# Optimization experiments

Measured on AMD Instinct MI355X. Metric: run time of the kernel, lower is better.

## Reference

```python
import jax, jax.numpy as jnp
import numpy as np

B, S, V, D, H, L, C = 64, 128, 50000, 300, 128, 20, 3
EPS = 1e-8


def lstm(x, w_ih, w_hh, b):
    # x: (B,S,D) -> outputs (B,S,H); torch gate order i,f,g,o
    xg = jnp.einsum('bsd,gd->bsg', x, w_ih) + b  # (B,S,4H)
    Hh = w_hh.shape[1]

    def step(carry, xt):
        hprev, cprev = carry
        g = xt + hprev @ w_hh.T
        i, f, gg, o = jnp.split(g, 4, axis=-1)
        c = jax.nn.sigmoid(f) * cprev + jax.nn.sigmoid(i) * jnp.tanh(gg)
        hnew = jax.nn.sigmoid(o) * jnp.tanh(c)
        return (hnew, c), hnew

    z = jnp.zeros((x.shape[0], Hh), x.dtype)
    _, hs = jax.lax.scan(step, (z, z), xg.transpose(1, 0, 2))
    return hs.transpose(1, 0, 2)


def bilstm(x, wih_f, whh_f, b_f, wih_b, whh_b, b_b):
    fwd = lstm(x, wih_f, whh_f, b_f)
    bwd = jnp.flip(lstm(jnp.flip(x, 1), wih_b, whh_b, b_b), 1)
    return jnp.concatenate([fwd, bwd], axis=-1)


def safe_div(prod, norm):
    # matches module's cosine_similarity eps handling
    return prod / jnp.where(norm > EPS, norm, EPS)


def full_matching(p1, p2, w):
    # p1: (B,S,H), p2: (B,H), w: (H,L) -> (B,S,L)
    v1 = p1[:, :, :, None] * w          # (B,S,H,L)
    v2 = p2[:, :, None] * w             # (B,H,L)
    dot = jnp.einsum('bshl,bhl->bsl', v1, v2)
    n1 = jnp.linalg.norm(v1, axis=2)    # (B,S,L)
    n2 = jnp.linalg.norm(v2, axis=1)    # (B,L)
    return dot / (jnp.maximum(n1, EPS) * jnp.maximum(n2, EPS)[:, None, :])


def maxpool_matching(p1, p2, w):
    v1 = p1[..., None] * w              # (B,S,H,L)
    v2 = p2[..., None] * w              # (B,T,H,L)
    prod = jnp.einsum('bshl,bthl->blst', v1, v2)
    n1 = jnp.linalg.norm(v1, axis=2)    # (B,S,L)
    n2 = jnp.linalg.norm(v2, axis=2)    # (B,T,L)
    deno = jnp.einsum('bsl,btl->blst', n1, n2)
    return safe_div(prod, deno).max(axis=3).transpose(0, 2, 1)  # (B,S,L)


def _wcos(a, b, w):
    # F.cosine_similarity over hidden dim of a*w vs b*w -> (B,S,L)
    va = a[..., None] * w
    vb = b[..., None] * w
    dot = jnp.einsum('bshl,bshl->bsl', va, vb)
    na = jnp.linalg.norm(va, axis=2)
    nb = jnp.linalg.norm(vb, axis=2)
    return dot / (jnp.maximum(na, EPS) * jnp.maximum(nb, EPS))


def attentive_matching(p1, p2, w_att, w_max):
    n1 = jnp.linalg.norm(p1, axis=2, keepdims=True)   # (B,S,1)
    n2 = jnp.linalg.norm(p2, axis=2, keepdims=True)   # (B,T,1)
    alpha = safe_div(jnp.einsum('bsh,bth->bst', p1, p2),
                     n1 * n2.transpose(0, 2, 1))       # (B,S,T)
    max_idx = jnp.argmax(alpha, axis=2)                # (B,S)
    h_mat = jnp.einsum('bst,bth->bsh', alpha, p2)
    resultant = h_mat / alpha.sum(axis=2, keepdims=True)
    result_match = _wcos(resultant, p1, w_att)
    out_mat = jnp.take_along_axis(p2, max_idx[..., None], axis=1)  # (B,S,H)
    result_max = _wcos(out_mat, p1, w_max)
    return result_match, result_max


def setup_inputs() -> dict:
    key = jax.random.key(0)
    ks = jax.random.split(key, 32)
    g = lambda k, shp, s=0.05: (jax.random.normal(k, shp, jnp.float32) * s)
    inp = {
        'emb': g(ks[0], (V, D), 0.1),
        'ctx_wih_f': g(ks[1], (4 * H, D)), 'ctx_whh_f': g(ks[2], (4 * H, H)), 'ctx_b_f': jnp.zeros((4 * H,), jnp.float32),
        'ctx_wih_b': g(ks[3], (4 * H, D)), 'ctx_whh_b': g(ks[4], (4 * H, H)), 'ctx_b_b': jnp.zeros((4 * H,), jnp.float32),
        'agg_wih_f': g(ks[5], (4 * H, 8 * L)), 'agg_whh_f': g(ks[6], (4 * H, H)), 'agg_b_f': jnp.zeros((4 * H,), jnp.float32),
        'agg_wih_b': g(ks[7], (4 * H, 8 * L)), 'agg_whh_b': g(ks[8], (4 * H, H)), 'agg_b_b': jnp.zeros((4 * H,), jnp.float32),
        'pW1': g(ks[9], (2 * H, 4 * H)), 'pb1': jnp.zeros((2 * H,), jnp.float32),
        'pW2': g(ks[10], (C, 2 * H)), 'pb2': jnp.zeros((C,), jnp.float32),
        'p': jax.random.randint(ks[11], (B, S), 0, V),
        'h': jax.random.randint(ks[12], (B, S), 0, V),
    }
    for i in range(1, 9):
        inp[f'w{i}'] = g(ks[12 + i], (H, L), 0.5)
    return inp


def reference(emb, ctx_wih_f, ctx_whh_f, ctx_b_f, ctx_wih_b, ctx_whh_b, ctx_b_b,
              agg_wih_f, agg_whh_f, agg_b_f, agg_wih_b, agg_whh_b, agg_b_b,
              pW1, pb1, pW2, pb2, w1, w2, w3, w4, w5, w6, w7, w8, p, h):
    p1_in = emb[p]
    p2_in = emb[h]
    c1 = bilstm(p1_in, ctx_wih_f, ctx_whh_f, ctx_b_f, ctx_wih_b, ctx_whh_b, ctx_b_b)
    c2 = bilstm(p2_in, ctx_wih_f, ctx_whh_f, ctx_b_f, ctx_wih_b, ctx_whh_b, ctx_b_b)
    c1f, c1b = jnp.split(c1, 2, axis=-1)
    c2f, c2b = jnp.split(c2, 2, axis=-1)

    match_p1_f = full_matching(c1f, c2f[:, -1], w1)
    match_p1_b = full_matching(c1b, c2b[:, -1], w2)
    match_p2_f = full_matching(c2f, c1f[:, -1], w1)
    match_p2_b = full_matching(c2b, c1b[:, -1], w2)

    maxm_p1_f = maxpool_matching(c1f, c2f, w3)
    maxm_p1_b = maxpool_matching(c1b, c2b, w4)
    maxm_p2_f = maxpool_matching(c2f, c1f, w3)
    maxm_p2_b = maxpool_matching(c2b, c1b, w4)

    att_p1_f, attm_p1_f = attentive_matching(c1f, c2f, w5, w7)
    att_p1_b, attm_p1_b = attentive_matching(c1b, c2b, w6, w8)
    att_p2_f, attm_p2_f = attentive_matching(c2f, c1f, w5, w7)
    att_p2_b, attm_p2_b = attentive_matching(c2b, c1b, w6, w8)

    aggr_p1 = jnp.concatenate([match_p1_f, match_p1_b, maxm_p1_f, maxm_p1_b,
                               att_p1_f, att_p1_b, attm_p1_f, attm_p1_b], axis=2)
    aggr_p2 = jnp.concatenate([match_p2_f, match_p2_b, maxm_p2_f, maxm_p2_b,
                               att_p2_f, att_p2_b, attm_p2_f, attm_p2_b], axis=2)

    agg_p = bilstm(aggr_p1, agg_wih_f, agg_whh_f, agg_b_f, agg_wih_b, agg_whh_b, agg_b_b)
    agg_h = bilstm(aggr_p2, agg_wih_f, agg_whh_f, agg_b_f, agg_wih_b, agg_whh_b, agg_b_b)
    out = jnp.concatenate([agg_p[:, -1], agg_h[:, -1]], axis=1)  # (B,4H)
    out = jax.nn.relu(out @ pW1.T + pb1) @ pW2.T + pb2
    return out
```

## Files before the change

kernel.cpp:

```cpp
#include <hip/hip_runtime.h>
#include <math.h>

#define B_  64
#define S_  128
#define H_  128
#define D_  300
#define L_  20
#define G4  512
#define SH  (S_*H_)
#define BSH ((size_t)B_*SH)
#define EPSV 1e-8f

typedef __attribute__((ext_vector_type(8))) short bshort8;
typedef __attribute__((ext_vector_type(4))) float f32x4;

__device__ __forceinline__ unsigned fmap(float f){
  unsigned u = __float_as_uint(f);
  return (u & 0x80000000u) ? ~u : (u | 0x80000000u);
}
__device__ __forceinline__ float funmap(unsigned u){
  return __uint_as_float((u & 0x80000000u) ? (u & 0x7fffffffu) : ~u);
}
__device__ __forceinline__ float fsigm(float x){ return 1.f/(1.f+__expf(-x)); }
__device__ __forceinline__ float ftanh(float x){ return 1.f - 2.f/(__expf(2.f*x)+1.f); }
__device__ __forceinline__ float dot4(float4 a, float4 b){
  return a.x*b.x + a.y*b.y + a.z*b.z + a.w*b.w;
}
__device__ __forceinline__ float blane(float v, int k){
  return __int_as_float(__builtin_amdgcn_readlane(__float_as_int(v), k));
}
__device__ __forceinline__ unsigned short f2bf(float f){
  unsigned u = __float_as_uint(f);
  unsigned r = u + 0x7fffu + ((u >> 16) & 1u);
  return (unsigned short)(r >> 16);
}
__device__ __forceinline__ float bf2f(unsigned short us){
  return __uint_as_float(((unsigned)us) << 16);
}
__device__ __forceinline__ int swz64(int row, int h){
  return (row << 6) + ((((h >> 2) ^ ((row >> 3) & 15)) << 2) | (h & 3));
}
__device__ __forceinline__ int swz128(int row, int h){
  return (row << 7) + ((((h >> 2) ^ ((row >> 3) & 15)) << 2) | (h & 3));
}
__device__ __forceinline__ int bswz(int row, int slot){
  return (row << 7) + (((slot ^ (row & 15)) << 3));
}
__device__ __forceinline__ void cvt8(float4 a0, float4 a1, int4& hi, int4& lo){
  float v[8] = {a0.x, a0.y, a0.z, a0.w, a1.x, a1.y, a1.z, a1.w};
  unsigned short h[8], l[8];
  #pragma unroll
  for (int i = 0; i < 8; i++) {
    h[i] = f2bf(v[i]);
    float d = v[i] - bf2f(h[i]);
    l[i] = f2bf(d);
  }
  hi = make_int4((unsigned)h[0] | ((unsigned)h[1] << 16), (unsigned)h[2] | ((unsigned)h[3] << 16),
                 (unsigned)h[4] | ((unsigned)h[5] << 16), (unsigned)h[6] | ((unsigned)h[7] << 16));
  lo = make_int4((unsigned)l[0] | ((unsigned)l[1] << 16), (unsigned)l[2] | ((unsigned)l[3] << 16),
                 (unsigned)l[4] | ((unsigned)l[5] << 16), (unsigned)l[6] | ((unsigned)l[7] << 16));
}

__global__ void k_embed(const float* __restrict__ emb, const int* __restrict__ p,
                        const int* __restrict__ h, float* __restrict__ x1,
                        float* __restrict__ x2)
{
  int row = blockIdx.x;
  const int* idx = blockIdx.y ? h : p;
  float* x = blockIdx.y ? x2 : x1;
  int tok = idx[row];
  const float* src = emb + (size_t)tok * D_;
  float* dst = x + (size_t)row * D_;
  for (int d = threadIdx.x; d < D_; d += blockDim.x) dst[d] = src[d];
}

template<int K>
__global__ __launch_bounds__(512, 1) void gemm_abt(
    const float* __restrict__ A0, const float* __restrict__ A1,
    const float* __restrict__ W0, const float* __restrict__ W1,
    const float* __restrict__ b0, const float* __restrict__ b1,
    float* __restrict__ Cbase, int M, int N)
{
  int q = blockIdx.z;
  const float* A = (q >> 1) ? A1 : A0;
  const float* W = (q & 1) ? W1 : W0;
  const float* bias = (q & 1) ? b1 : b0;
  float* Cm = Cbase + (size_t)q * M * N;

  __shared__ __align__(16) short AsH[128 * 32];
  __shared__ __align__(16) short AsL[128 * 32];
  __shared__ __align__(16) short WsH[128 * 32];
  __shared__ __align__(16) short WsL[128 * 32];

  int t = threadIdx.x;
  int w = t >> 6, lane = t & 63;
  int r = lane & 15, g = lane >> 4;
  int m0 = blockIdx.x * 128, n0 = blockIdx.y * 128;
  int mbase = (w & 1) * 64;
  int nbase = (w >> 1) * 32;

  f32x4 acc[4][2];
  #pragma unroll
  for (int i = 0; i < 4; i++)
    #pragma unroll
    for (int j = 0; j < 2; j++) acc[i][j] = (f32x4){0.f, 0.f, 0.f, 0.f};

  int srow = t >> 2, skc = t & 3;
  int soff = srow * 32 + ((skc ^ ((srow >> 1) & 3)) << 3);

  #pragma unroll 1
  for (int k0 = 0; k0 < K; k0 += 32) {
    {
      int gk = k0 + (skc << 3);
      float4 z = make_float4(0.f, 0.f, 0.f, 0.f);
      float4 a0v = z, a1v = z, w0v = z, w1v = z;
      if (gk < K) {
        a0v = *(const float4*)&A[(size_t)(m0 + srow) * K + gk];
        w0v = *(const float4*)&W[(size_t)(n0 + srow) * K + gk];
      }
      if (gk + 4 < K) {
        a1v = *(const float4*)&A[(size_t)(m0 + srow) * K + gk + 4];
        w1v = *(const float4*)&W[(size_t)(n0 + srow) * K + gk + 4];
      }
      int4 hi, lo;
      cvt8(a0v, a1v, hi, lo);
      *(int4*)&AsH[soff] = hi; *(int4*)&AsL[soff] = lo;
      cvt8(w0v, w1v, hi, lo);
      *(int4*)&WsH[soff] = hi; *(int4*)&WsL[soff] = lo;
    }
    __syncthreads();
    bshort8 ah[4], al[4], bh[2], bl[2];
    #pragma unroll
    for (int i = 0; i < 4; i++) {
      int R = mbase + i * 16 + r;
      int off = R * 32 + ((g ^ ((R >> 1) & 3)) << 3);
      ah[i] = *(const bshort8*)&AsH[off];
      al[i] = *(const bshort8*)&AsL[off];
    }
    #pragma unroll
    for (int j = 0; j < 2; j++) {
      int R = nbase + j * 16 + r;
      int off = R * 32 + ((g ^ ((R >> 1) & 3)) << 3);
      bh[j] = *(const bshort8*)&WsH[off];
      bl[j] = *(const bshort8*)&WsL[off];
    }
    #pragma unroll
    for (int i = 0; i < 4; i++)
      #pragma unroll
      for (int j = 0; j < 2; j++) {
        acc[i][j] = __builtin_amdgcn_mfma_f32_16x16x32_bf16(ah[i], bh[j], acc[i][j], 0, 0, 0);
        acc[i][j] = __builtin_amdgcn_mfma_f32_16x16x32_bf16(ah[i], bl[j], acc[i][j], 0, 0, 0);
        acc[i][j] = __builtin_amdgcn_mfma_f32_16x16x32_bf16(al[i], bh[j], acc[i][j], 0, 0, 0);
      }
    __syncthreads();
  }
  #pragma unroll
  for (int j = 0; j < 2; j++) {
    int gcol = n0 + nbase + j * 16 + r;
    float bv = bias[gcol];
    #pragma unroll
    for (int i = 0; i < 4; i++) {
      #pragma unroll
      for (int rg = 0; rg < 4; rg++) {
        int grow = m0 + mbase + i * 16 + g * 4 + rg;
        Cm[(size_t)grow * N + gcol] = acc[i][j][rg] + bv;
      }
    }
  }
}

__global__ __launch_bounds__(512, 1) void k_lstm(const float* __restrict__ xg,
    const float* __restrict__ whhF, const float* __restrict__ whhB,
    float* __restrict__ hs)
{
  int b = blockIdx.x, q = blockIdx.y, dir = q & 1;
  const float* whh = dir ? whhB : whhF;
  const float* xgq = xg + ((size_t)(q * B_ + b)) * (S_ * G4);
  float* out = hs + ((size_t)(q * B_ + b)) * SH;
  int t = threadIdx.x;
  int j = t & 255;
  int kh = t >> 8;
  int lane = t & 63;

  float2 w2[64];
  {
    const float* wr0 = whh + (size_t)j * 128 + kh * 64;
    const float* wr1 = whh + (size_t)(j + 256) * 128 + kh * 64;
    #pragma unroll
    for (int k = 0; k < 64; k += 4) {
      float4 v0 = *(const float4*)(wr0 + k);
      float4 v1 = *(const float4*)(wr1 + k);
      w2[k]     = make_float2(v0.x, v1.x);
      w2[k + 1] = make_float2(v0.y, v1.y);
      w2[k + 2] = make_float2(v0.z, v1.z);
      w2[k + 3] = make_float2(v0.w, v1.w);
    }
  }
  __shared__ float hsm[128];
  __shared__ float csm[128];
  __shared__ float gsm[2][512];
  if (t < 128) { hsm[t] = 0.f; csm[t] = 0.f; }
  __syncthreads();

  float hreg = 0.f;
  float xn0 = 0.f, xn1 = 0.f;
  if (kh == 0) {
    int t0 = dir ? (S_ - 1) : 0;
    xn0 = xgq[(size_t)t0 * G4 + j];
    xn1 = xgq[(size_t)t0 * G4 + j + 256];
  }

  for (int st = 0; st < S_; st++) {
    int tt = dir ? (S_ - 1 - st) : st;
    float x0 = xn0, x1 = xn1;
    if (kh == 0) {
      int stn = (st + 1 < S_) ? st + 1 : st;
      int ttn = dir ? (S_ - 1 - stn) : stn;
      xn0 = xgq[(size_t)ttn * G4 + j];
      xn1 = xgq[(size_t)ttn * G4 + j + 256];
    }
    float a0x = (kh == 0) ? x0 : 0.f, a0y = (kh == 0) ? x1 : 0.f;
    float a1x = 0.f, a1y = 0.f, a2x = 0.f, a2y = 0.f, a3x = 0.f, a3y = 0.f;
    #pragma unroll
    for (int k = 0; k < 64; k += 4) {
      float s0 = blane(hreg, k);
      float s1 = blane(hreg, k + 1);
      float s2 = blane(hreg, k + 2);
      float s3 = blane(hreg, k + 3);
      a0x += w2[k].x * s0;     a0y += w2[k].y * s0;
      a1x += w2[k + 1].x * s1; a1y += w2[k + 1].y * s1;
      a2x += w2[k + 2].x * s2; a2y += w2[k + 2].y * s2;
      a3x += w2[k + 3].x * s3; a3y += w2[k + 3].y * s3;
    }
    gsm[kh][j]       = (a0x + a1x) + (a2x + a3x);
    gsm[kh][j + 256] = (a0y + a1y) + (a2y + a3y);
    __syncthreads();
    if (t < 128) {
      float gi = gsm[0][t]       + gsm[1][t];
      float gf = gsm[0][128 + t] + gsm[1][128 + t];
      float gg = gsm[0][256 + t] + gsm[1][256 + t];
      float go = gsm[0][384 + t] + gsm[1][384 + t];
      float ig = fsigm(gi);
      float fg = fsigm(gf);
      float gv = ftanh(gg);
      float og = fsigm(go);
      float c = fg * csm[t] + ig * gv;
      float hn = og * ftanh(c);
      csm[t] = c; hsm[t] = hn;
      out[(size_t)tt * H_ + t] = hn;
    }
    __syncthreads();
    hreg = hsm[kh * 64 + lane];
  }
}

__global__ __launch_bounds__(256) void k_full(const float* __restrict__ C,
    const float* __restrict__ w1, const float* __restrict__ w2,
    float* __restrict__ ag1, float* __restrict__ ag2)
{
  int b = blockIdx.x, q = blockIdx.y, dir = q & 1;
  const float* p1  = C + (size_t)q * BSH + (size_t)b * SH;
  const float* p2l = C + (size_t)((q + 2) & 3) * BSH + (size_t)b * SH + (size_t)(S_ - 1) * H_;
  const float* w = dir ? w2 : w1;
  float* out = (q < 2 ? ag1 : ag2) + (size_t)b * S_ * 160;

  __shared__ float p1s[SH];
  __shared__ float ws2[H_][L_];
  __shared__ float p2s[H_];
  __shared__ float n2s[L_];
  int t = threadIdx.x;
  for (int i = t; i < SH; i += 256) p1s[i] = p1[i];
  for (int i = t; i < H_ * L_; i += 256) { float v = w[i]; ws2[i / L_][i % L_] = v * v; }
  if (t < H_) p2s[t] = p2l[t];
  __syncthreads();
  if (t < L_) {
    float s = 0.f;
    for (int hh = 0; hh < H_; hh++) { float v = p2s[hh]; s += v * v * ws2[hh][t]; }
    n2s[t] = sqrtf(s);
  }
  __syncthreads();
  for (int i = t; i < S_ * L_; i += 256) {
    int s = i / L_, l = i % L_;
    const float* pr = p1s + s * H_;
    float dot = 0.f, n1 = 0.f;
    for (int hh = 0; hh < H_; hh++) {
      float a = pr[hh], ww = ws2[hh][l];
      dot += a * p2s[hh] * ww;
      n1 += a * a * ww;
    }
    n1 = sqrtf(n1);
    out[(size_t)s * 160 + dir * L_ + l] = dot / (fmaxf(n1, EPSV) * fmaxf(n2s[l], EPSV));
  }
}

__global__ __launch_bounds__(512, 1) void k_maxpool(const float* __restrict__ C,
    const float* __restrict__ w3, const float* __restrict__ w4,
    float* __restrict__ ag1, float* __restrict__ ag2)
{
  int b = blockIdx.x, dir = blockIdx.y, lh = blockIdx.z;
  const float* p1 = C + (size_t)(0 + dir) * BSH + (size_t)b * SH;
  const float* p2 = C + (size_t)(2 + dir) * BSH + (size_t)b * SH;
  const float* w = dir ? w4 : w3;

  __shared__ __align__(16) short P1b[128 * 128];
  __shared__ __align__(16) short P2b[128 * 128];
  __shared__ __align__(16) short Ab[128 * 128];
  __shared__ float w2s[128 * 10];
  __shared__ float n1s[128], n2s[128];
  __shared__ unsigned mx2u[128];

  int t = threadIdx.x;
  int wv = t >> 6, lane = t & 63;
  int g = lane >> 4, col = lane & 15;

  for (int i = t; i < 8192; i += 512) {
    int row = i >> 6, hp = i & 63;
    int phys = bswz(row, hp >> 2) + ((hp & 3) << 1);
    float2 v1 = *(const float2*)&p1[(row << 7) + (hp << 1)];
    float2 v2 = *(const float2*)&p2[(row << 7) + (hp << 1)];
    *(unsigned*)&P1b[phys] = (unsigned)f2bf(v1.x) | ((unsigned)f2bf(v1.y) << 16);
    *(unsigned*)&P2b[phys] = (unsigned)f2bf(v2.x) | ((unsigned)f2bf(v2.y) << 16);
  }
  for (int i = t; i < 128 * 10; i += 512) {
    int hh = i / 10, lq = i % 10;
    float wv_ = w[hh * L_ + lh * 10 + lq];
    w2s[i] = wv_ * wv_;
  }
  __syncthreads();

  #pragma unroll 1
  for (int lq = 0; lq < 10; lq++) {
    int lout = lh * 10 + lq;
    for (int i = t; i < 8192; i += 512) {
      int row = i >> 6, hp = i & 63;
      int phys = bswz(row, hp >> 2) + ((hp & 3) << 1);
      unsigned u = *(const unsigned*)&P1b[phys];
      float lo = bf2f((unsigned short)(u & 0xffffu)) * w2s[(hp << 1) * 10 + lq];
      float hi = bf2f((unsigned short)(u >> 16))     * w2s[((hp << 1) + 1) * 10 + lq];
      *(unsigned*)&Ab[phys] = (unsigned)f2bf(lo) | ((unsigned)f2bf(hi) << 16);
    }
    {
      int s = t >> 2, part = t & 3;
      float s1 = 0.f, s2 = 0.f;
      #pragma unroll 1
      for (int hp = part * 16; hp < part * 16 + 16; hp++) {
        int phys = bswz(s, hp >> 2) + ((hp & 3) << 1);
        unsigned u1 = *(const unsigned*)&P1b[phys];
        unsigned u2 = *(const unsigned*)&P2b[phys];
        float wlo = w2s[(hp << 1) * 10 + lq];
        float whi = w2s[((hp << 1) + 1) * 10 + lq];
        float a = bf2f((unsigned short)(u1 & 0xffffu)), bb = bf2f((unsigned short)(u1 >> 16));
        float c2 = bf2f((unsigned short)(u2 & 0xffffu)), d2 = bf2f((unsigned short)(u2 >> 16));
        s1 += a * a * wlo + bb * bb * whi;
        s2 += c2 * c2 * wlo + d2 * d2 * whi;
      }
      s1 += __shfl_xor(s1, 1, 64); s1 += __shfl_xor(s1, 2, 64);
      s2 += __shfl_xor(s2, 1, 64); s2 += __shfl_xor(s2, 2, 64);
      if (part == 0) { n1s[s] = sqrtf(s1); n2s[s] = sqrtf(s2); }
    }
    if (t < 128) mx2u[t] = fmap(-3.4e38f);
    __syncthreads();

    {
      int mrow = (wv << 4) + col;
      f32x4 acc0 = {0,0,0,0}, acc1 = {0,0,0,0}, acc2 = {0,0,0,0}, acc3 = {0,0,0,0};
      f32x4 acc4 = {0,0,0,0}, acc5 = {0,0,0,0}, acc6 = {0,0,0,0}, acc7 = {0,0,0,0};
      #pragma unroll 1
      for (int k0 = 0; k0 < 128; k0 += 32) {
        int slot = ((k0 >> 3) + g) ^ col;
        bshort8 av = *(const bshort8*)&Ab[(mrow << 7) + (slot << 3)];
        bshort8 bv0 = *(const bshort8*)&P2b[((0 << 4) + col << 7) + (slot << 3)];
        bshort8 bv1 = *(const bshort8*)&P2b[(((1 << 4) + col) << 7) + (slot << 3)];
        bshort8 bv2 = *(const bshort8*)&P2b[(((2 << 4) + col) << 7) + (slot << 3)];
        bshort8 bv3 = *(const bshort8*)&P2b[(((3 << 4) + col) << 7) + (slot << 3)];
        bshort8 bv4 = *(const bshort8*)&P2b[(((4 << 4) + col) << 7) + (slot << 3)];
        bshort8 bv5 = *(const bshort8*)&P2b[(((5 << 4) + col) << 7) + (slot << 3)];
        bshort8 bv6 = *(const bshort8*)&P2b[(((6 << 4) + col) << 7) + (slot << 3)];
        bshort8 bv7 = *(const bshort8*)&P2b[(((7 << 4) + col) << 7) + (slot << 3)];
        acc0 = __builtin_amdgcn_mfma_f32_16x16x32_bf16(av, bv0, acc0, 0, 0, 0);
        acc1 = __builtin_amdgcn_mfma_f32_16x16x32_bf16(av, bv1, acc1, 0, 0, 0);
        acc2 = __builtin_amdgcn_mfma_f32_16x16x32_bf16(av, bv2, acc2, 0, 0, 0);
        acc3 = __builtin_amdgcn_mfma_f32_16x16x32_bf16(av, bv3, acc3, 0, 0, 0);
        acc4 = __builtin_amdgcn_mfma_f32_16x16x32_bf16(av, bv4, acc4, 0, 0, 0);
        acc5 = __builtin_amdgcn_mfma_f32_16x16x32_bf16(av, bv5, acc5, 0, 0, 0);
        acc6 = __builtin_amdgcn_mfma_f32_16x16x32_bf16(av, bv6, acc6, 0, 0, 0);
        acc7 = __builtin_amdgcn_mfma_f32_16x16x32_bf16(av, bv7, acc7, 0, 0, 0);
      }
      float n1v[4];
      #pragma unroll
      for (int r = 0; r < 4; r++) n1v[r] = n1s[(wv << 4) + (g << 2) + r];
      float rm[4] = {-3.4e38f, -3.4e38f, -3.4e38f, -3.4e38f};
      float cm[8];
      f32x4 accs[8] = {acc0, acc1, acc2, acc3, acc4, acc5, acc6, acc7};
      #pragma unroll
      for (int c = 0; c < 8; c++) {
        float n2v = n2s[(c << 4) + col];
        float cmx = -3.4e38f;
        #pragma unroll
        for (int r = 0; r < 4; r++) {
          float deno = n1v[r] * n2v;
          float cs = accs[c][r] / (deno > EPSV ? deno : EPSV);
          rm[r] = fmaxf(rm[r], cs);
          cmx = fmaxf(cmx, cs);
        }
        cm[c] = cmx;
      }
      #pragma unroll
      for (int m = 1; m < 16; m <<= 1)
        #pragma unroll
        for (int r = 0; r < 4; r++) rm[r] = fmaxf(rm[r], __shfl_xor(rm[r], m, 64));
      if (col == 0) {
        #pragma unroll
        for (int r = 0; r < 4; r++) {
          int srow = (wv << 4) + (g << 2) + r;
          ag1[(size_t)b * S_ * 160 + (size_t)srow * 160 + 40 + dir * L_ + lout] = rm[r];
        }
      }
      #pragma unroll
      for (int c = 0; c < 8; c++) {
        cm[c] = fmaxf(cm[c], __shfl_xor(cm[c], 16, 64));
        cm[c] = fmaxf(cm[c], __shfl_xor(cm[c], 32, 64));
      }
      if (lane < 16) {
        #pragma unroll
        for (int c = 0; c < 8; c++) atomicMax(&mx2u[(c << 4) + lane], fmap(cm[c]));
      }
    }
    __syncthreads();
    if (t < 128)
      ag2[(size_t)b * S_ * 160 + (size_t)t * 160 + 40 + dir * L_ + lout] = funmap(mx2u[t]);
    __syncthreads();
  }
}

__global__ __launch_bounds__(256, 1) void k_alpha(const float* __restrict__ C,
                                                  float* __restrict__ alpha)
{
  int b = blockIdx.x, dir = blockIdx.y;
  const float* p1 = C + (size_t)(0 + dir) * BSH + (size_t)b * SH;
  const float* p2 = C + (size_t)(2 + dir) * BSH + (size_t)b * SH;
  __shared__ __align__(16) float a1[128 * 64];
  __shared__ __align__(16) float a2[128 * 64];
  __shared__ float n1p[128], n2p[128];
  int t = threadIdx.x, tx = t & 15, ty = t >> 4;
  float acc[8][8] = {};

  for (int pass = 0; pass < 2; pass++) {
    int h0 = pass << 6;
    for (int i = t; i < 128 * 64; i += 256) {
      int row = i >> 6, hh = i & 63;
      int off = swz64(row, hh);
      a1[off] = p1[(size_t)row * H_ + h0 + hh];
      a2[off] = p2[(size_t)row * H_ + h0 + hh];
    }
    __syncthreads();
    {
      int r = t & 127;
      const float* a = (t < 128) ? a1 : a2;
      float s = 0.f;
      #pragma unroll 1
      for (int f = 0; f < 16; f++) {
        float4 v = *(const float4*)&a[(r << 6) + ((f ^ ((r >> 3) & 15)) << 2)];
        s += dot4(v, v);
      }
      float* np = (t < 128) ? n1p : n2p;
      if (pass == 0) np[r] = s; else np[r] += s;
    }
    #pragma unroll 1
    for (int f = 0; f < 16; f++) {
      int cx = ((f ^ ty) << 2);
      int cy = ((f ^ tx) << 2);
      float4 x[8], y[8];
      #pragma unroll
      for (int i = 0; i < 8; i++) x[i] = *(const float4*)&a1[((8 * ty + i) << 6) + cx];
      #pragma unroll
      for (int j = 0; j < 8; j++) y[j] = *(const float4*)&a2[((8 * tx + j) << 6) + cy];
      #pragma unroll
      for (int i = 0; i < 8; i++)
        #pragma unroll
        for (int j = 0; j < 8; j++) acc[i][j] += dot4(x[i], y[j]);
    }
    __syncthreads();
  }
  float inv1[8], inv2[8];
  #pragma unroll
  for (int i = 0; i < 8; i++) inv1[i] = 1.f / fmaxf(sqrtf(n1p[8 * ty + i]), EPSV);
  #pragma unroll
  for (int j = 0; j < 8; j++) inv2[j] = 1.f / fmaxf(sqrtf(n2p[8 * tx + j]), EPSV);
  float* outp = alpha + ((size_t)dir * B_ + b) * SH;
  #pragma unroll
  for (int i = 0; i < 8; i++) {
    int ss = 8 * ty + i;
    float s1 = inv1[i];
    float4 o0 = make_float4(acc[i][0] * s1 * inv2[0], acc[i][1] * s1 * inv2[1],
                            acc[i][2] * s1 * inv2[2], acc[i][3] * s1 * inv2[3]);
    float4 o1 = make_float4(acc[i][4] * s1 * inv2[4], acc[i][5] * s1 * inv2[5],
                            acc[i][6] * s1 * inv2[6], acc[i][7] * s1 * inv2[7]);
    *(float4*)&outp[(size_t)ss * S_ + 8 * tx] = o0;
    *(float4*)&outp[(size_t)ss * S_ + 8 * tx + 4] = o1;
  }
}

__global__ __launch_bounds__(256, 1) void k_att(const float* __restrict__ C,
    const float* __restrict__ alpha,
    const float* __restrict__ w5, const float* __restrict__ w6,
    const float* __restrict__ w7, const float* __restrict__ w8,
    float* __restrict__ ag1, float* __restrict__ ag2)
{
  int b = blockIdx.x, q = blockIdx.y, dir = q & 1;
  const float* p1  = C + (size_t)q * BSH + (size_t)b * SH;
  const float* m2g = C + (size_t)((q + 2) & 3) * BSH + (size_t)b * SH;
  const float* wa = dir ? w6 : w5;
  const float* wm = dir ? w8 : w7;
  const float* ain = alpha + ((size_t)dir * B_ + b) * SH;
  float* out = (q < 2 ? ag1 : ag2) + (size_t)b * S_ * 160;
  bool tr = (q >= 2);

  __shared__ __align__(16) float A[128 * 128];
  __shared__ __align__(16) float M2T[128 * 128];
  __shared__ __align__(16) float waT[20 * 128];
  __shared__ __align__(16) float wmT[20 * 128];
  __shared__ float rowsum[128];
  __shared__ int   midx[128];
  int t = threadIdx.x, tx = t & 15, ty = t >> 4;

  for (int i = t; i < SH; i += 256) {
    int r = i >> 7, c = i & 127;
    float av = ain[i];
    if (tr) A[swz128(c, r)] = av; else A[swz128(r, c)] = av;
    M2T[swz128(c, r)] = m2g[i];
  }
  for (int i = t; i < H_ * L_; i += 256) {
    int hh = i / L_, l = i % L_;
    float v = wa[i]; waT[l * 128 + hh] = v * v;
    float u = wm[i]; wmT[l * 128 + hh] = u * u;
  }
  __syncthreads();

  if (t < 128) {
    float sum = 0.f, best = -3.4e38f; int bi = 0;
    #pragma unroll 1
    for (int f = 0; f < 32; f++) {
      float4 v = *(const float4*)&A[(t << 7) + (((f ^ ((t >> 3) & 15)) & 31) << 2)];
      sum += v.x + v.y + v.z + v.w;
      int k = f << 2;
      if (v.x > best) { best = v.x; bi = k; }
      if (v.y > best) { best = v.y; bi = k + 1; }
      if (v.z > best) { best = v.z; bi = k + 2; }
      if (v.w > best) { best = v.w; bi = k + 3; }
    }
    rowsum[t] = sum; midx[t] = bi;
  }
  __syncthreads();

  float acc[8][8] = {};
  #pragma unroll 1
  for (int f = 0; f < 32; f++) {
    int cx = (((f ^ ty) & 31) << 2);
    int cy = (((f ^ tx) & 31) << 2);
    float4 x[8], y[8];
    #pragma unroll
    for (int i = 0; i < 8; i++) x[i] = *(const float4*)&A[((8 * ty + i) << 7) + cx];
    #pragma unroll
    for (int j = 0; j < 8; j++) y[j] = *(const float4*)&M2T[((8 * tx + j) << 7) + cy];
    #pragma unroll
    for (int i = 0; i < 8; i++)
      #pragma unroll
      for (int j = 0; j < 8; j++) acc[i][j] += dot4(x[i], y[j]);
  }
  __syncthreads();
  {
    float rinv[8];
    #pragma unroll
    for (int i = 0; i < 8; i++) rinv[i] = 1.f / rowsum[8 * ty + i];
    #pragma unroll
    for (int i = 0; i < 8; i++) {
      int row = 8 * ty + i;
      int f0 = (2 * tx) ^ ((row >> 3) & 15);
      int f1 = (2 * tx + 1) ^ ((row >> 3) & 15);
      float4 o0 = make_float4(acc[i][0] * rinv[i], acc[i][1] * rinv[i],
                              acc[i][2] * rinv[i], acc[i][3] * rinv[i]);
      float4 o1 = make_float4(acc[i][4] * rinv[i], acc[i][5] * rinv[i],
                              acc[i][6] * rinv[i], acc[i][7] * rinv[i]);
      *(float4*)&A[(row << 7) + (f0 << 2)] = o0;
      *(float4*)&A[(row << 7) + (f1 << 2)] = o1;
    }
  }
  __syncthreads();

  {
    int s = t >> 1, l0 = (t & 1) * 10;
    int mi = midx[s];
    const float* m2r = m2g + (size_t)mi * H_;
    const float* p1r = p1 + (size_t)s * H_;
    float dA[10] = {}, nA[10] = {}, bA[10] = {};
    float dM[10] = {}, nM[10] = {}, bM[10] = {};
    #pragma unroll 1
    for (int f = 0; f < 32; f++) {
      float4 pv = *(const float4*)&p1r[f << 2];
      float4 mv = *(const float4*)&m2r[f << 2];
      float4 av = *(const float4*)&A[(s << 7) + (((f ^ ((s >> 3) & 15)) & 31) << 2)];
      float4 ap = make_float4(av.x*pv.x, av.y*pv.y, av.z*pv.z, av.w*pv.w);
      float4 a2 = make_float4(av.x*av.x, av.y*av.y, av.z*av.z, av.w*av.w);
      float4 p2 = make_float4(pv.x*pv.x, pv.y*pv.y, pv.z*pv.z, pv.w*pv.w);
      float4 mp = make_float4(mv.x*pv.x, mv.y*pv.y, mv.z*pv.z, mv.w*pv.w);
      float4 m2 = make_float4(mv.x*mv.x, mv.y*mv.y, mv.z*mv.z, mv.w*mv.w);
      #pragma unroll
      for (int l = 0; l < 10; l++) {
        float4 wv = *(const float4*)&waT[(l0 + l) * 128 + (f << 2)];
        dA[l] += dot4(ap, wv); nA[l] += dot4(a2, wv); bA[l] += dot4(p2, wv);
        float4 uv = *(const float4*)&wmT[(l0 + l) * 128 + (f << 2)];
        dM[l] += dot4(mp, uv); nM[l] += dot4(m2, uv); bM[l] += dot4(p2, uv);
      }
    }
    #pragma unroll
    for (int l = 0; l < 10; l++) {
      int ll = l0 + l;
      out[(size_t)s * 160 + 80  + dir * L_ + ll] =
          dA[l] / (fmaxf(sqrtf(nA[l]), EPSV) * fmaxf(sqrtf(bA[l]), EPSV));
      out[(size_t)s * 160 + 120 + dir * L_ + ll] =
          dM[l] / (fmaxf(sqrtf(nM[l]), EPSV) * fmaxf(sqrtf(bM[l]), EPSV));
    }
  }
}

__global__ __launch_bounds__(256) void k_final(const float* __restrict__ Cc,
    const float* __restrict__ pW1, const float* __restrict__ pb1,
    const float* __restrict__ pW2, const float* __restrict__ pb2,
    float* __restrict__ out)
{
  int b = blockIdx.x, t = threadIdx.x;
  __shared__ float cat[512];
  __shared__ float hid[256];
  if (t < 128) {
    cat[t]       = Cc[(size_t)(0 * B_ + b) * SH + (size_t)(S_ - 1) * H_ + t];
    cat[128 + t] = Cc[(size_t)(1 * B_ + b) * SH + (size_t)(S_ - 1) * H_ + t];
    cat[256 + t] = Cc[(size_t)(2 * B_ + b) * SH + (size_t)(S_ - 1) * H_ + t];
    cat[384 + t] = Cc[(size_t)(3 * B_ + b) * SH + (size_t)(S_ - 1) * H_ + t];
  }
  __syncthreads();
  float a = pb1[t];
  for (int k = 0; k < 512; k++) a += cat[k] * pW1[(size_t)t * 512 + k];
  hid[t] = fmaxf(a, 0.f);
  __syncthreads();
  if (t < 3) {
    float o = pb2[t];
    for (int k = 0; k < 256; k++) o += hid[k] * pW2[(size_t)t * 256 + k];
    out[(size_t)b * 3 + t] = o;
  }
}

extern "C" void kernel_launch(void* const* d_in, const int* in_sizes, int n_in,
                              void* d_out, int out_size, void* d_ws, size_t ws_size,
                              hipStream_t stream)
{
  const float* emb    = (const float*)d_in[0];
  const float* cwih_f = (const float*)d_in[1];
  const float* cwhh_f = (const float*)d_in[2];
  const float* cb_f   = (const float*)d_in[3];
  const float* cwih_b = (const float*)d_in[4];
  const float* cwhh_b = (const float*)d_in[5];
  const float* cb_b   = (const float*)d_in[6];
  const float* awih_f = (const float*)d_in[7];
  const float* awhh_f = (const float*)d_in[8];
  const float* ab_f   = (const float*)d_in[9];
  const float* awih_b = (const float*)d_in[10];
  const float* awhh_b = (const float*)d_in[11];
  const float* ab_b   = (const float*)d_in[12];
  const float* pW1    = (const float*)d_in[13];
  const float* pb1    = (const float*)d_in[14];
  const float* pW2    = (const float*)d_in[15];
  const float* pb2    = (const float*)d_in[16];
  const int*   pidx   = (const int*)d_in[17];
  const int*   hidx   = (const int*)d_in[18];
  const float* w1 = (const float*)d_in[19];
  const float* w2 = (const float*)d_in[20];
  const float* w3 = (const float*)d_in[21];
  const float* w4 = (const float*)d_in[22];
  const float* w5 = (const float*)d_in[23];
  const float* w6 = (const float*)d_in[24];
  const float* w7 = (const float*)d_in[25];
  const float* w8 = (const float*)d_in[26];

  float* ws = (float*)d_ws;
  float* XG   = ws;
  float* X1   = ws + 16777216;
  float* X2   = X1 + 2457600;
  float* ALPH = X1;
  float* AG1  = ws + 16777216 + 2097152;
  float* AG2  = AG1 + (size_t)B_ * S_ * 160;
  float* CC   = ws + 21692416;

  k_embed<<<dim3(B_ * S_, 2), 256, 0, stream>>>(emb, pidx, hidx, X1, X2);
  gemm_abt<D_><<<dim3(64, 4, 4), 512, 0, stream>>>(X1, X2, cwih_f, cwih_b, cb_f, cb_b,
                                                   XG, B_ * S_, G4);
  k_lstm<<<dim3(B_, 4), 512, 0, stream>>>(XG, cwhh_f, cwhh_b, CC);
  k_full<<<dim3(B_, 4), 256, 0, stream>>>(CC, w1, w2, AG1, AG2);
  k_maxpool<<<dim3(B_, 2, 2), 512, 0, stream>>>(CC, w3, w4, AG1, AG2);
  k_alpha<<<dim3(B_, 2), 256, 0, stream>>>(CC, ALPH);
  k_att<<<dim3(B_, 4), 256, 0, stream>>>(CC, ALPH, w5, w6, w7, w8, AG1, AG2);
  gemm_abt<8 * L_><<<dim3(64, 4, 4), 512, 0, stream>>>(AG1, AG2, awih_f, awih_b, ab_f, ab_b,
                                                       XG, B_ * S_, G4);
  k_lstm<<<dim3(B_, 4), 512, 0, stream>>>(XG, awhh_f, awhh_b, CC);
  k_final<<<dim3(B_), 256, 0, stream>>>(CC, pW1, pb1, pW2, pb2, (float*)d_out);
}
```

Before: 612.9 us.

## Fuse embedding gather into input GEMM and full-matching into attentive kernel

The input-projection GEMM now reads embedding rows directly through the token indices, so the separate embedding kernel and its intermediate X1/X2 buffers go away. The full-matching cosine computation moves into the tail of the attentive-matching kernel, which drops the k_full launch and its shared-memory staging of p1. This removes two launches and one round trip of the embedded activations through global memory. In exchange, the fused full-matching reads the weights straight from global memory with a strided pattern and adds serial work to k_att.

```diff
diff --git a/kernel.cpp b/kernel.cpp
--- a/kernel.cpp
+++ b/kernel.cpp
@@ -61,28 +61,16 @@
                  (unsigned)l[4] | ((unsigned)l[5] << 16), (unsigned)l[6] | ((unsigned)l[7] << 16));
 }
 
-__global__ void k_embed(const float* __restrict__ emb, const int* __restrict__ p,
-                        const int* __restrict__ h, float* __restrict__ x1,
-                        float* __restrict__ x2)
-{
-  int row = blockIdx.x;
-  const int* idx = blockIdx.y ? h : p;
-  float* x = blockIdx.y ? x2 : x1;
-  int tok = idx[row];
-  const float* src = emb + (size_t)tok * D_;
-  float* dst = x + (size_t)row * D_;
-  for (int d = threadIdx.x; d < D_; d += blockDim.x) dst[d] = src[d];
-}
-
-template<int K>
+template<int K, bool GATHER>
 __global__ __launch_bounds__(512, 1) void gemm_abt(
     const float* __restrict__ A0, const float* __restrict__ A1,
+    const int* __restrict__ idxP, const int* __restrict__ idxH,
+    const float* __restrict__ emb,
     const float* __restrict__ W0, const float* __restrict__ W1,
     const float* __restrict__ b0, const float* __restrict__ b1,
     float* __restrict__ Cbase, int M, int N)
 {
   int q = blockIdx.z;
-  const float* A = (q >> 1) ? A1 : A0;
   const float* W = (q & 1) ? W1 : W0;
   const float* bias = (q & 1) ? b1 : b0;
   float* Cm = Cbase + (size_t)q * M * N;
@@ -107,6 +95,15 @@
 
   int srow = t >> 2, skc = t & 3;
   int soff = srow * 32 + ((skc ^ ((srow >> 1) & 3)) << 3);
+
+  const float* arow;
+  if (GATHER) {
+    const int* idx = (q >> 1) ? idxH : idxP;
+    arow = emb + (size_t)idx[m0 + srow] * K;
+  } else {
+    arow = ((q >> 1) ? A1 : A0) + (size_t)(m0 + srow) * K;
+  }
+  const float* wrow = W + (size_t)(n0 + srow) * K;
 
   #pragma unroll 1
   for (int k0 = 0; k0 < K; k0 += 32) {
@@ -115,12 +112,12 @@
       float4 z = make_float4(0.f, 0.f, 0.f, 0.f);
       float4 a0v = z, a1v = z, w0v = z, w1v = z;
       if (gk < K) {
-        a0v = *(const float4*)&A[(size_t)(m0 + srow) * K + gk];
-        w0v = *(const float4*)&W[(size_t)(n0 + srow) * K + gk];
+        a0v = *(const float4*)&arow[gk];
+        w0v = *(const float4*)&wrow[gk];
       }
       if (gk + 4 < K) {
-        a1v = *(const float4*)&A[(size_t)(m0 + srow) * K + gk + 4];
-        w1v = *(const float4*)&W[(size_t)(n0 + srow) * K + gk + 4];
+        a1v = *(const float4*)&arow[gk + 4];
+        w1v = *(const float4*)&wrow[gk + 4];
       }
       int4 hi, lo;
       cvt8(a0v, a1v, hi, lo);
@@ -251,45 +248,6 @@
     }
     __syncthreads();
     hreg = hsm[kh * 64 + lane];
-  }
-}
-
-__global__ __launch_bounds__(256) void k_full(const float* __restrict__ C,
-    const float* __restrict__ w1, const float* __restrict__ w2,
-    float* __restrict__ ag1, float* __restrict__ ag2)
-{
-  int b = blockIdx.x, q = blockIdx.y, dir = q & 1;
-  const float* p1  = C + (size_t)q * BSH + (size_t)b * SH;
-  const float* p2l = C + (size_t)((q + 2) & 3) * BSH + (size_t)b * SH + (size_t)(S_ - 1) * H_;
-  const float* w = dir ? w2 : w1;
-  float* out = (q < 2 ? ag1 : ag2) + (size_t)b * S_ * 160;
-
-  __shared__ float p1s[SH];
-  __shared__ float ws2[H_][L_];
-  __shared__ float p2s[H_];
-  __shared__ float n2s[L_];
-  int t = threadIdx.x;
-  for (int i = t; i < SH; i += 256) p1s[i] = p1[i];
-  for (int i = t; i < H_ * L_; i += 256) { float v = w[i]; ws2[i / L_][i % L_] = v * v; }
-  if (t < H_) p2s[t] = p2l[t];
-  __syncthreads();
-  if (t < L_) {
-    float s = 0.f;
-    for (int hh = 0; hh < H_; hh++) { float v = p2s[hh]; s += v * v * ws2[hh][t]; }
-    n2s[t] = sqrtf(s);
-  }
-  __syncthreads();
-  for (int i = t; i < S_ * L_; i += 256) {
-    int s = i / L_, l = i % L_;
-    const float* pr = p1s + s * H_;
-    float dot = 0.f, n1 = 0.f;
-    for (int hh = 0; hh < H_; hh++) {
-      float a = pr[hh], ww = ws2[hh][l];
-      dot += a * p2s[hh] * ww;
-      n1 += a * a * ww;
-    }
-    n1 = sqrtf(n1);
-    out[(size_t)s * 160 + dir * L_ + l] = dot / (fmaxf(n1, EPSV) * fmaxf(n2s[l], EPSV));
   }
 }
 
@@ -505,6 +463,7 @@
     const float* __restrict__ alpha,
     const float* __restrict__ w5, const float* __restrict__ w6,
     const float* __restrict__ w7, const float* __restrict__ w8,
+    const float* __restrict__ w1, const float* __restrict__ w2,
     float* __restrict__ ag1, float* __restrict__ ag2)
 {
   int b = blockIdx.x, q = blockIdx.y, dir = q & 1;
@@ -620,6 +579,36 @@
           dA[l] / (fmaxf(sqrtf(nA[l]), EPSV) * fmaxf(sqrtf(bA[l]), EPSV));
       out[(size_t)s * 160 + 120 + dir * L_ + ll] =
           dM[l] / (fmaxf(sqrtf(nM[l]), EPSV) * fmaxf(sqrtf(bM[l]), EPSV));
+    }
+  }
+
+  {
+    int s = t >> 1, l0f = (t & 1) * 10;
+    const float* wf = dir ? w2 : w1;
+    const float* p1r = p1 + (size_t)s * H_;
+    const float* p2l = m2g + (size_t)(S_ - 1) * H_;
+    float dF[10] = {}, n1F[10] = {}, n2F[10] = {};
+    #pragma unroll 1
+    for (int f = 0; f < 32; f++) {
+      float4 pv = *(const float4*)&p1r[f << 2];
+      float4 qv = *(const float4*)&p2l[f << 2];
+      #pragma unroll
+      for (int l = 0; l < 10; l++) {
+        int ll = l0f + l;
+        float wa0 = wf[(f * 4 + 0) * L_ + ll]; wa0 *= wa0;
+        float wa1 = wf[(f * 4 + 1) * L_ + ll]; wa1 *= wa1;
+        float wa2 = wf[(f * 4 + 2) * L_ + ll]; wa2 *= wa2;
+        float wa3 = wf[(f * 4 + 3) * L_ + ll]; wa3 *= wa3;
+        dF[l]  += pv.x*qv.x*wa0 + pv.y*qv.y*wa1 + pv.z*qv.z*wa2 + pv.w*qv.w*wa3;
+        n1F[l] += pv.x*pv.x*wa0 + pv.y*pv.y*wa1 + pv.z*pv.z*wa2 + pv.w*pv.w*wa3;
+        n2F[l] += qv.x*qv.x*wa0 + qv.y*qv.y*wa1 + qv.z*qv.z*wa2 + qv.w*qv.w*wa3;
+      }
+    }
+    #pragma unroll
+    for (int l = 0; l < 10; l++) {
+      int ll = l0f + l;
+      out[(size_t)s * 160 + dir * L_ + ll] =
+          dF[l] / (fmaxf(sqrtf(n1F[l]), EPSV) * fmaxf(sqrtf(n2F[l]), EPSV));
     }
   }
 }
@@ -684,23 +673,22 @@
 
   float* ws = (float*)d_ws;
   float* XG   = ws;
-  float* X1   = ws + 16777216;
-  float* X2   = X1 + 2457600;
-  float* ALPH = X1;
+  float* ALPH = ws + 16777216;
   float* AG1  = ws + 16777216 + 2097152;
   float* AG2  = AG1 + (size_t)B_ * S_ * 160;
   float* CC   = ws + 21692416;
 
-  k_embed<<<dim3(B_ * S_, 2), 256, 0, stream>>>(emb, pidx, hidx, X1, X2);
-  gemm_abt<D_><<<dim3(64, 4, 4), 512, 0, stream>>>(X1, X2, cwih_f, cwih_b, cb_f, cb_b,
-                                                   XG, B_ * S_, G4);
+  gemm_abt<D_, true><<<dim3(64, 4, 4), 512, 0, stream>>>(
+      nullptr, nullptr, pidx, hidx, emb, cwih_f, cwih_b, cb_f, cb_b,
+      XG, B_ * S_, G4);
   k_lstm<<<dim3(B_, 4), 512, 0, stream>>>(XG, cwhh_f, cwhh_b, CC);
-  k_full<<<dim3(B_, 4), 256, 0, stream>>>(CC, w1, w2, AG1, AG2);
   k_maxpool<<<dim3(B_, 2, 2), 512, 0, stream>>>(CC, w3, w4, AG1, AG2);
   k_alpha<<<dim3(B_, 2), 256, 0, stream>>>(CC, ALPH);
-  k_att<<<dim3(B_, 4), 256, 0, stream>>>(CC, ALPH, w5, w6, w7, w8, AG1, AG2);
-  gemm_abt<8 * L_><<<dim3(64, 4, 4), 512, 0, stream>>>(AG1, AG2, awih_f, awih_b, ab_f, ab_b,
-                                                       XG, B_ * S_, G4);
+  k_att<<<dim3(B_, 4), 256, 0, stream>>>(CC, ALPH, w5, w6, w7, w8, w1, w2,
+                                         AG1, AG2);
+  gemm_abt<8 * L_, false><<<dim3(64, 4, 4), 512, 0, stream>>>(
+      AG1, AG2, nullptr, nullptr, nullptr, awih_f, awih_b, ab_f, ab_b,
+      XG, B_ * S_, G4);
   k_lstm<<<dim3(B_, 4), 512, 0, stream>>>(XG, awhh_f, awhh_b, CC);
   k_final<<<dim3(B_), 256, 0, stream>>>(CC, pW1, pb1, pW2, pb2, (float*)d_out);
 }
```

New measurement: 584.5 us. -4.6%, faster.
